# Kernel tuning notes

Measured on AMD Instinct MI355X. Metric: run time of the kernel, lower is better.

## Reference

```python
import jax, jax.numpy as jnp
import numpy as np

B = 1_000_000   # reflections
K = 16_384      # groups
E = 64          # encoder_out
H = 64          # hidden_dim


def setup_inputs() -> dict:
    key = jax.random.key(0)
    ks = jax.random.split(key, 12)
    x = jax.random.normal(ks[0], (B, E), dtype=jnp.float32)
    gl = jax.random.randint(ks[1], (B,), 0, K)
    # guarantee every group id 0..K-1 appears, so torch.unique == arange(K)
    gl = gl.at[:K].set(jnp.arange(K))
    s = 0.05
    W1 = jax.random.normal(ks[2], (E, H), jnp.float32) * s
    b1 = jax.random.normal(ks[3], (H,), jnp.float32) * s
    W2 = jax.random.normal(ks[4], (H, H), jnp.float32) * s
    b2 = jax.random.normal(ks[5], (H,), jnp.float32) * s
    W3 = jax.random.normal(ks[6], (H, H), jnp.float32) * s
    b3 = jax.random.normal(ks[7], (H,), jnp.float32) * s
    w_mu = jax.random.normal(ks[8], (H, 1), jnp.float32) * s
    b_mu = jnp.full((1,), -6.9, jnp.float32)   # log_tau_init
    w_lv = jax.random.normal(ks[9], (H, 1), jnp.float32) * s
    b_lv = jnp.full((1,), -2.0, jnp.float32)
    return {"x": x, "group_labels": gl, "W1": W1, "b1": b1, "W2": W2, "b2": b2,
            "W3": W3, "b3": b3, "w_mu": w_mu, "b_mu": b_mu, "w_lv": w_lv, "b_lv": b_lv}


def reference(x, group_labels, W1, b1, W2, b2, W3, b3, w_mu, b_mu, w_lv, b_lv):
    # phi: Linear -> SiLU -> Linear -> SiLU
    z = jax.nn.silu(jax.nn.silu(x @ W1 + b1) @ W2 + b2)          # (B, H)
    # segment mean by group (math-equivalent to the dense one-hot matmul)
    counts = jax.ops.segment_sum(jnp.ones((z.shape[0],), z.dtype),
                                 group_labels, num_segments=K)    # (K,)
    gsum = jax.ops.segment_sum(z, group_labels, num_segments=K)   # (K, H)
    group_features = gsum / counts[:, None]
    # rho + heads
    h = jax.nn.silu(group_features @ W3 + b3)                     # (K, H)
    mu = (h @ w_mu + b_mu)[:, 0]                                  # (K,)
    logvar = jnp.clip((h @ w_lv + b_lv)[:, 0], -10.0, 4.0)        # (K,)
    std = jnp.exp(0.5 * logvar)
    eps = jax.random.normal(jax.random.key(42), std.shape, std.dtype)
    log_tau = mu + std * eps                                      # reparam sample
    tau_group = jnp.exp(log_tau)
    # unique_groups == arange(K) by construction -> searchsorted is identity
    tau_per_refl = tau_group[group_labels][:, None]               # (B, 1)
    log_tau_per_refl = log_tau[group_labels][:, None]             # (B, 1)
    return (mu, logvar, tau_per_refl, log_tau_per_refl)
```

## Files before the change

### kernel.cpp

```cpp
#include <hip/hip_runtime.h>

#define BN 1000000
#define KN 16384
#define HN 64
#define TPB 512
#define NW  8
#define CHROWS 256
#define NB  512
#define NCHUNK ((BN + CHROWS - 1) / CHROWS)

typedef __bf16 bf16x8 __attribute__((ext_vector_type(8)));
typedef float  f32x4  __attribute__((ext_vector_type(4)));
typedef unsigned short u16x8 __attribute__((ext_vector_type(8)));

__device__ __forceinline__ unsigned short f2bf(float f) {
    return __builtin_bit_cast(unsigned short, (__bf16)f);
}
__device__ __forceinline__ float bf2f(unsigned short b) {
    return (float)__builtin_bit_cast(__bf16, b);
}
__device__ __forceinline__ float silu_f(float v) {
    return v * __builtin_amdgcn_rcpf(1.0f + __expf(-v));
}
__device__ __forceinline__ f32x4 mfma16(bf16x8 a, bf16x8 b, f32x4 c) {
    return __builtin_amdgcn_mfma_f32_16x16x32_bf16(a, b, c, 0, 0, 0);
}

__device__ __forceinline__ float erfinv_xla(float x) {
    float w = -log1pf(-x * x);
    float p;
    if (w < 5.0f) {
        w -= 2.5f;
        p = 2.81022636e-08f;
        p = fmaf(p, w, 3.43273939e-07f);
        p = fmaf(p, w, -3.5233877e-06f);
        p = fmaf(p, w, -4.39150654e-06f);
        p = fmaf(p, w, 0.00021858087f);
        p = fmaf(p, w, -0.00125372503f);
        p = fmaf(p, w, -0.00417768164f);
        p = fmaf(p, w, 0.246640727f);
        p = fmaf(p, w, 1.50140941f);
    } else {
        w = sqrtf(w) - 3.0f;
        p = -0.000200214257f;
        p = fmaf(p, w, 0.000100950558f);
        p = fmaf(p, w, 0.00134934322f);
        p = fmaf(p, w, -0.00367342844f);
        p = fmaf(p, w, 0.00573950773f);
        p = fmaf(p, w, -0.0076224613f);
        p = fmaf(p, w, 0.00943887047f);
        p = fmaf(p, w, 1.00167406f);
        p = fmaf(p, w, 2.83297682f);
    }
    return p * x;
}

__device__ __forceinline__ float jax_eps16384(int gid) {
    const unsigned k0 = 0u, k1 = 42u, k2 = 0x1BD11BDAu ^ 0u ^ 42u;
    unsigned x0 = 0u + k0;
    unsigned x1 = (unsigned)gid + k1;
#define TF_RND(r) { x0 += x1; x1 = (x1 << (r)) | (x1 >> (32 - (r))); x1 ^= x0; }
    TF_RND(13) TF_RND(15) TF_RND(26) TF_RND(6)  x0 += k1; x1 += k2 + 1u;
    TF_RND(17) TF_RND(29) TF_RND(16) TF_RND(24) x0 += k2; x1 += k0 + 2u;
    TF_RND(13) TF_RND(15) TF_RND(26) TF_RND(6)  x0 += k0; x1 += k1 + 3u;
    TF_RND(17) TF_RND(29) TF_RND(16) TF_RND(24) x0 += k1; x1 += k2 + 4u;
    TF_RND(13) TF_RND(15) TF_RND(26) TF_RND(6)  x0 += k2; x1 += k0 + 5u;
#undef TF_RND
    unsigned bits = x0 ^ x1;
    float f = __uint_as_float((bits >> 9) | 0x3f800000u) - 1.0f;
    const float mn = -0.99999994f;
    float u = fmaxf(f * 2.0f + mn, mn);
    return 1.41421354f * erfinv_xla(u);
}

__global__ __launch_bounds__(256) void k_count(const int* __restrict__ gl,
                                               int* __restrict__ counts,
                                               float4* __restrict__ gz) {
    int i = blockIdx.x * 256 + threadIdx.x;
    const float4 z4 = make_float4(0.f, 0.f, 0.f, 0.f);
    for (int j = i; j < KN * HN / 4; j += 250112) gz[j] = z4;
    if (i < BN / 4) {
        int4 g = ((const int4*)gl)[i];
        atomicAdd(&counts[g.x], 1); atomicAdd(&counts[g.y], 1);
        atomicAdd(&counts[g.z], 1); atomicAdd(&counts[g.w], 1);
    }
}

__global__ __launch_bounds__(1024) void k_scan(const int* __restrict__ counts, int* __restrict__ cursor) {
    __shared__ int wtot[16];
    const int t = threadIdx.x, lane = t & 63, wv = t >> 6;
    const int4* c4 = (const int4*)counts;
    int4 q0 = c4[t * 4], q1 = c4[t * 4 + 1], q2 = c4[t * 4 + 2], q3 = c4[t * 4 + 3];
    int c[16] = {q0.x, q0.y, q0.z, q0.w, q1.x, q1.y, q1.z, q1.w,
                 q2.x, q2.y, q2.z, q2.w, q3.x, q3.y, q3.z, q3.w};
    int loc[16], s = 0;
    #pragma unroll
    for (int i = 0; i < 16; ++i) { loc[i] = s; s += c[i]; }
    const int own = s;
    #pragma unroll
    for (int off = 1; off < 64; off <<= 1) {
        int v = __shfl_up(s, off);
        if (lane >= off) s += v;
    }
    if (lane == 63) wtot[wv] = s;
    __syncthreads();
    int wbase = 0;
    #pragma unroll
    for (int w = 0; w < 16; ++w) wbase += (w < wv) ? wtot[w] : 0;
    const int ebase = wbase + s - own;
    int o[16];
    #pragma unroll
    for (int i = 0; i < 16; ++i) o[i] = ebase + loc[i];
    int4* o4 = (int4*)cursor;
    o4[t * 4]     = make_int4(o[0],  o[1],  o[2],  o[3]);
    o4[t * 4 + 1] = make_int4(o[4],  o[5],  o[6],  o[7]);
    o4[t * 4 + 2] = make_int4(o[8],  o[9],  o[10], o[11]);
    o4[t * 4 + 3] = make_int4(o[12], o[13], o[14], o[15]);
}

__global__ __launch_bounds__(256) void k_scatter(const int* __restrict__ gl, int* __restrict__ cursor,
                                                 int2* __restrict__ spk) {
    int i = blockIdx.x * 256 + threadIdx.x;
    if (i < BN / 4) {
        int4 g = ((const int4*)gl)[i];
        int r = i * 4;
        int p0 = atomicAdd(&cursor[g.x], 1); spk[p0] = make_int2(r,     g.x);
        int p1 = atomicAdd(&cursor[g.y], 1); spk[p1] = make_int2(r + 1, g.y);
        int p2 = atomicAdd(&cursor[g.z], 1); spk[p2] = make_int2(r + 2, g.z);
        int p3 = atomicAdd(&cursor[g.w], 1); spk[p3] = make_int2(r + 3, g.w);
    }
}

__global__ __launch_bounds__(TPB, 4) void k_phase1(
    const float* __restrict__ x, const int2* __restrict__ spk,
    const float* __restrict__ W1, const float* __restrict__ b1,
    const float* __restrict__ W2, const float* __restrict__ b2,
    float* __restrict__ gsum)
{
    __shared__ __align__(16) unsigned short w1t[64 * 64];
    __shared__ __align__(16) unsigned short w2t[64 * 64];
    __shared__ __align__(16) unsigned short xh[NW][32 * 64];
    __shared__ float b1s[64], b2s[64];
    __shared__ int sg_s[NW][32];

    const int t = threadIdx.x;
    const int wv = t >> 6, lane = t & 63;
    const int lj = lane & 15, lg = lane >> 4;

    {
        const float4* W1v = (const float4*)W1;
        const float4* W2v = (const float4*)W2;
        #pragma unroll
        for (int i = 0; i < 2; ++i) {
            int e4 = i * TPB + t;
            int k  = e4 >> 4;
            int j0 = (e4 & 15) * 4;
            float4 a = W1v[e4];
            float4 b = W2v[e4];
            float av[4] = {a.x, a.y, a.z, a.w};
            float bv[4] = {b.x, b.y, b.z, b.w};
            #pragma unroll
            for (int c = 0; c < 4; ++c) {
                int j = j0 + c;
                int off = j * 128 + ((2 * k) ^ ((j & 7) << 4));
                *(unsigned short*)((char*)w1t + off) = f2bf(av[c]);
                *(unsigned short*)((char*)w2t + off) = f2bf(bv[c]);
            }
        }
        if (t < 64) { b1s[t] = b1[t]; b2s[t] = b2[t]; }
    }
    __syncthreads();

    float bc1[4], bc2[4];
    #pragma unroll
    for (int ct = 0; ct < 4; ++ct) { bc1[ct] = b1s[ct * 16 + lj]; bc2[ct] = b2s[ct * 16 + lj]; }

    unsigned short* myx = &xh[wv][0];
    int2 rsA[2], rsB[2];

    auto load_spk = [&](int c, int2 (&dst)[2]) {
        int cc = c < NCHUNK - 1 ? c : NCHUNK - 1;
        #pragma unroll
        for (int rt = 0; rt < 2; ++rt) {
            int r = cc * CHROWS + wv * 32 + rt * 16 + lj;
            dst[rt] = spk[r < BN ? r : BN - 1];
        }
    };

    auto iter = [&](int2 (&CUR)[2], int2 (&NXT)[2], int c) {
        float4 xr[2][4];
        #pragma unroll
        for (int rt = 0; rt < 2; ++rt) {
            const float* xp = x + (size_t)CUR[rt].x * 64 + lg * 8;
            xr[rt][0] = *(const float4*)(xp);
            xr[rt][1] = *(const float4*)(xp + 4);
            xr[rt][2] = *(const float4*)(xp + 32);
            xr[rt][3] = *(const float4*)(xp + 36);
        }
        load_spk(c + NB, NXT);
        if (lg == 0) {
            #pragma unroll
            for (int rt = 0; rt < 2; ++rt) {
                int r = c * CHROWS + wv * 32 + rt * 16 + lj;
                sg_s[wv][rt * 16 + lj] = (r < BN) ? CUR[rt].y : -1;
            }
        }
        bf16x8 af[2][2];
        #pragma unroll
        for (int rt = 0; rt < 2; ++rt)
            #pragma unroll
            for (int kk = 0; kk < 2; ++kk) {
                float4 a = xr[rt][kk * 2], b = xr[rt][kk * 2 + 1];
                u16x8 u;
                u[0] = f2bf(a.x); u[1] = f2bf(a.y); u[2] = f2bf(a.z); u[3] = f2bf(a.w);
                u[4] = f2bf(b.x); u[5] = f2bf(b.y); u[6] = f2bf(b.z); u[7] = f2bf(b.w);
                af[rt][kk] = __builtin_bit_cast(bf16x8, u);
            }

        f32x4 acc[2][4];
        #pragma unroll
        for (int a = 0; a < 2; ++a)
            #pragma unroll
            for (int b = 0; b < 4; ++b) acc[a][b] = f32x4{0.f, 0.f, 0.f, 0.f};
        #pragma unroll
        for (int kk = 0; kk < 2; ++kk) {
            const int kbyte = kk * 64 + lg * 16;
            bf16x8 bw[4];
            #pragma unroll
            for (int ct = 0; ct < 4; ++ct) {
                int row = ct * 16 + lj;
                bw[ct] = *(const bf16x8*)((char*)w1t + row * 128 + (kbyte ^ ((row & 7) << 4)));
            }
            #pragma unroll
            for (int rt = 0; rt < 2; ++rt)
                #pragma unroll
                for (int ct = 0; ct < 4; ++ct)
                    acc[rt][ct] = mfma16(af[rt][kk], bw[ct], acc[rt][ct]);
        }
        #pragma unroll
        for (int rt = 0; rt < 2; ++rt) {
            #pragma unroll
            for (int ct = 0; ct < 4; ++ct) {
                f32x4 v = acc[rt][ct];
                #pragma unroll
                for (int rg = 0; rg < 4; ++rg) {
                    int row = rt * 16 + lg * 4 + rg;
                    int col = ct * 16 + lj;
                    float h = silu_f(v[rg] + bc1[ct]);
                    int off = row * 128 + ((2 * col) ^ ((row & 7) << 4));
                    *(unsigned short*)((char*)myx + off) = f2bf(h);
                }
                acc[rt][ct] = f32x4{0.f, 0.f, 0.f, 0.f};
            }
        }
        #pragma unroll
        for (int kk = 0; kk < 2; ++kk) {
            const int kbyte = kk * 64 + lg * 16;
            bf16x8 bw[4];
            #pragma unroll
            for (int ct = 0; ct < 4; ++ct) {
                int row = ct * 16 + lj;
                bw[ct] = *(const bf16x8*)((char*)w2t + row * 128 + (kbyte ^ ((row & 7) << 4)));
            }
            #pragma unroll
            for (int rt = 0; rt < 2; ++rt) {
                int row = rt * 16 + lj;
                bf16x8 aw = *(const bf16x8*)((char*)myx + row * 128 + (kbyte ^ ((row & 7) << 4)));
                #pragma unroll
                for (int ct = 0; ct < 4; ++ct)
                    acc[rt][ct] = mfma16(aw, bw[ct], acc[rt][ct]);
            }
        }
        #pragma unroll
        for (int rt = 0; rt < 2; ++rt) {
            #pragma unroll
            for (int ct = 0; ct < 4; ++ct) {
                f32x4 v = acc[rt][ct];
                int col  = ct * 16 + lj;
                int row0 = rt * 16 + lg * 4;
                ushort4 pk;
                pk.x = f2bf(silu_f(v[0] + bc2[ct]));
                pk.y = f2bf(silu_f(v[1] + bc2[ct]));
                pk.z = f2bf(silu_f(v[2] + bc2[ct]));
                pk.w = f2bf(silu_f(v[3] + bc2[ct]));
                *(ushort4*)((char*)myx + col * 64 + ((2 * row0) ^ ((col & 3) << 4))) = pk;
            }
        }
        {
            const int c2 = lane;
            const char* zT = (const char*)myx;
            float vsum = 0.0f;
            int curg = -2;
            #pragma unroll
            for (int blk = 0; blk < 4; ++blk) {
                u16x8 v = *(const u16x8*)(zT + c2 * 64 + ((16 * blk) ^ ((c2 & 3) << 4)));
                int4 ga = *(const int4*)(&sg_s[wv][blk * 8]);
                int4 gb = *(const int4*)(&sg_s[wv][blk * 8 + 4]);
                int gs[8] = {ga.x, ga.y, ga.z, ga.w, gb.x, gb.y, gb.z, gb.w};
                #pragma unroll
                for (int j = 0; j < 8; ++j) {
                    int g = gs[j];
                    if (g != curg) {
                        if (curg >= 0) atomicAdd(&gsum[curg * 64 + c2], vsum);
                        vsum = 0.0f;
                        curg = g;
                    }
                    vsum += bf2f(v[j]);
                }
            }
            if (curg >= 0) atomicAdd(&gsum[curg * 64 + c2], vsum);
        }
    };

    int c = blockIdx.x;
    load_spk(c, rsA);
    while (true) {
        iter(rsA, rsB, c); c += NB; if (c >= NCHUNK) break;
        iter(rsB, rsA, c); c += NB; if (c >= NCHUNK) break;
    }
}

__global__ __launch_bounds__(64) void k_phase2(
    const float* __restrict__ gsum, const int* __restrict__ counts,
    const float* __restrict__ W3, const float* __restrict__ b3,
    const float* __restrict__ wmu, const float* __restrict__ bmu,
    const float* __restrict__ wlv, const float* __restrict__ blv,
    float* __restrict__ out, float* __restrict__ taug, float* __restrict__ ltaug)
{
    __shared__ __align__(16) float w3t[64 * 64];
    __shared__ float b3s[64], wmus[64], wlvs[64];
    const int t = threadIdx.x;
    for (int i = 0; i < 64; ++i) w3t[t * 64 + i] = W3[i * 64 + t];
    b3s[t] = b3[t]; wmus[t] = wmu[t]; wlvs[t] = wlv[t];
    __syncthreads();

    const int gid = blockIdx.x * 64 + t;
    const float inv = 1.0f / (float)counts[gid];
    float gf[64];
    #pragma unroll
    for (int i = 0; i < 16; ++i) {
        float4 v = *(const float4*)(gsum + (size_t)gid * 64 + i * 4);
        gf[i * 4 + 0] = v.x * inv; gf[i * 4 + 1] = v.y * inv;
        gf[i * 4 + 2] = v.z * inv; gf[i * 4 + 3] = v.w * inv;
    }
    float mu = bmu[0], lv = blv[0];
    for (int j = 0; j < 64; ++j) {
        float a = b3s[j];
        const float4* wr = (const float4*)(w3t + j * 64);
        #pragma unroll
        for (int k = 0; k < 16; ++k) {
            float4 wv = wr[k];
            a += gf[k * 4 + 0] * wv.x + gf[k * 4 + 1] * wv.y
               + gf[k * 4 + 2] * wv.z + gf[k * 4 + 3] * wv.w;
        }
        float h = silu_f(a);
        mu += h * wmus[j];
        lv += h * wlvs[j];
    }
    lv = fminf(fmaxf(lv, -10.0f), 4.0f);
    float sd  = __expf(0.5f * lv);
    float eps = jax_eps16384(gid);
    float lt  = mu + sd * eps;
    out[gid]      = mu;
    out[KN + gid] = lv;
    taug[gid]  = __expf(lt);
    ltaug[gid] = lt;
}

__global__ __launch_bounds__(256) void k_phase3(
    const int* __restrict__ gl, const float* __restrict__ taug,
    const float* __restrict__ ltaug, float* __restrict__ out)
{
    int i = blockIdx.x * 256 + threadIdx.x;
    if (i < BN / 4) {
        int4 g = ((const int4*)gl)[i];
        float4 tv = make_float4(taug[g.x],  taug[g.y],  taug[g.z],  taug[g.w]);
        float4 lv = make_float4(ltaug[g.x], ltaug[g.y], ltaug[g.z], ltaug[g.w]);
        ((float4*)(out + 2 * KN))[i]      = tv;
        ((float4*)(out + 2 * KN + BN))[i] = lv;
    }
}

extern "C" void kernel_launch(void* const* d_in, const int* in_sizes, int n_in,
                              void* d_out, int out_size, void* d_ws, size_t ws_size,
                              hipStream_t stream)
{
    const float* x   = (const float*)d_in[0];
    const int*   gl  = (const int*)d_in[1];
    const float* W1  = (const float*)d_in[2];
    const float* b1  = (const float*)d_in[3];
    const float* W2  = (const float*)d_in[4];
    const float* b2  = (const float*)d_in[5];
    const float* W3  = (const float*)d_in[6];
    const float* b3  = (const float*)d_in[7];
    const float* wmu = (const float*)d_in[8];
    const float* bmu = (const float*)d_in[9];
    const float* wlv = (const float*)d_in[10];
    const float* blv = (const float*)d_in[11];
    float* out = (float*)d_out;

    float* ws     = (float*)d_ws;
    float* gsum   = ws;
    int*   counts = (int*)(gsum + KN * HN);
    int*   cursor = counts + KN;
    float* taug   = (float*)(cursor + KN);
    float* ltaug  = taug + KN;
    int2*  spk    = (int2*)(ltaug + KN);

    hipMemsetAsync(counts, 0, (size_t)KN * sizeof(int), stream);

    const int nb4 = (BN / 4 + 255) / 256;
    k_count  <<<nb4, 256, 0, stream>>>(gl, counts, (float4*)gsum);
    k_scan   <<<1, 1024, 0, stream>>>(counts, cursor);
    k_scatter<<<nb4, 256, 0, stream>>>(gl, cursor, spk);
    k_phase1 <<<NB, TPB, 0, stream>>>(x, spk, W1, b1, W2, b2, gsum);
    k_phase2 <<<KN / 64, 64, 0, stream>>>(gsum, counts, W3, b3, wmu, bmu, wlv, blv, out, taug, ltaug);
    k_phase3 <<<nb4, 256, 0, stream>>>(gl, taug, ltaug, out);
}
```

Before: 233.8 us.

## Software-pipeline x row gathers one chunk ahead in phase1 MLP loop

Restructures the phase1 loop so the gathered x rows for the next chunk are loaded right after the current chunk's rows are converted to bf16, and sorted-index loads are prefetched two chunks ahead. Scheduling barriers pin these loads before the MFMA work so memory latency overlaps compute. It also reorders the weight fragment loads into pairs and reads biases from LDS instead of holding them in registers, to relieve register pressure. The cost is extra live registers for the prefetched x rows, which could hurt occupancy under the four-block launch bound.

```diff
diff --git a/kernel.cpp b/kernel.cpp
--- a/kernel.cpp
+++ b/kernel.cpp
@@ -2,11 +2,10 @@
 
 #define BN 1000000
 #define KN 16384
-#define HN 64
-#define TPB 512
-#define NW  8
+#define TPB1 512
+#define NW1 8
 #define CHROWS 256
-#define NB  512
+#define NB1 512
 #define NCHUNK ((BN + CHROWS - 1) / CHROWS)
 
 typedef __bf16 bf16x8 __attribute__((ext_vector_type(8)));
@@ -78,7 +77,7 @@
                                                float4* __restrict__ gz) {
     int i = blockIdx.x * 256 + threadIdx.x;
     const float4 z4 = make_float4(0.f, 0.f, 0.f, 0.f);
-    for (int j = i; j < KN * HN / 4; j += 250112) gz[j] = z4;
+    for (int j = i; j < KN * 64 / 4; j += 250112) gz[j] = z4;
     if (i < BN / 4) {
         int4 g = ((const int4*)gl)[i];
         atomicAdd(&counts[g.x], 1); atomicAdd(&counts[g.y], 1);
@@ -131,7 +130,7 @@
     }
 }
 
-__global__ __launch_bounds__(TPB, 4) void k_phase1(
+__global__ __launch_bounds__(TPB1, 4) void k_phase1(
     const float* __restrict__ x, const int2* __restrict__ spk,
     const float* __restrict__ W1, const float* __restrict__ b1,
     const float* __restrict__ W2, const float* __restrict__ b2,
@@ -139,9 +138,9 @@
 {
     __shared__ __align__(16) unsigned short w1t[64 * 64];
     __shared__ __align__(16) unsigned short w2t[64 * 64];
-    __shared__ __align__(16) unsigned short xh[NW][32 * 64];
+    __shared__ __align__(16) unsigned short xh[NW1][32 * 64];
     __shared__ float b1s[64], b2s[64];
-    __shared__ int sg_s[NW][32];
+    __shared__ int sg_s[NW1][32];
 
     const int t = threadIdx.x;
     const int wv = t >> 6, lane = t & 63;
@@ -152,7 +151,7 @@
         const float4* W2v = (const float4*)W2;
         #pragma unroll
         for (int i = 0; i < 2; ++i) {
-            int e4 = i * TPB + t;
+            int e4 = i * TPB1 + t;
             int k  = e4 >> 4;
             int j0 = (e4 & 15) * 4;
             float4 a = W1v[e4];
@@ -171,12 +170,9 @@
     }
     __syncthreads();
 
-    float bc1[4], bc2[4];
-    #pragma unroll
-    for (int ct = 0; ct < 4; ++ct) { bc1[ct] = b1s[ct * 16 + lj]; bc2[ct] = b2s[ct * 16 + lj]; }
-
     unsigned short* myx = &xh[wv][0];
-    int2 rsA[2], rsB[2];
+    int2   rsA[2], rsB[2];
+    float4 xr[2][4];
 
     auto load_spk = [&](int c, int2 (&dst)[2]) {
         int cc = c < NCHUNK - 1 ? c : NCHUNK - 1;
@@ -186,25 +182,18 @@
             dst[rt] = spk[r < BN ? r : BN - 1];
         }
     };
-
-    auto iter = [&](int2 (&CUR)[2], int2 (&NXT)[2], int c) {
-        float4 xr[2][4];
+    auto load_x = [&](const int2 (&src)[2]) {
         #pragma unroll
         for (int rt = 0; rt < 2; ++rt) {
-            const float* xp = x + (size_t)CUR[rt].x * 64 + lg * 8;
+            const float* xp = x + (size_t)src[rt].x * 64 + lg * 8;
             xr[rt][0] = *(const float4*)(xp);
             xr[rt][1] = *(const float4*)(xp + 4);
             xr[rt][2] = *(const float4*)(xp + 32);
             xr[rt][3] = *(const float4*)(xp + 36);
         }
-        load_spk(c + NB, NXT);
-        if (lg == 0) {
-            #pragma unroll
-            for (int rt = 0; rt < 2; ++rt) {
-                int r = c * CHROWS + wv * 32 + rt * 16 + lj;
-                sg_s[wv][rt * 16 + lj] = (r < BN) ? CUR[rt].y : -1;
-            }
-        }
+    };
+
+    auto iter = [&](int2 (&CUR)[2], int2 (&NXT)[2], int c) {
         bf16x8 af[2][2];
         #pragma unroll
         for (int rt = 0; rt < 2; ++rt)
@@ -216,6 +205,17 @@
                 u[4] = f2bf(b.x); u[5] = f2bf(b.y); u[6] = f2bf(b.z); u[7] = f2bf(b.w);
                 af[rt][kk] = __builtin_bit_cast(bf16x8, u);
             }
+        if (lg == 0) {
+            #pragma unroll
+            for (int rt = 0; rt < 2; ++rt) {
+                int r = c * CHROWS + wv * 32 + rt * 16 + lj;
+                sg_s[wv][rt * 16 + lj] = (r < BN) ? CUR[rt].y : -1;
+            }
+        }
+        __builtin_amdgcn_sched_barrier(0);
+        load_x(NXT);
+        load_spk(c + 2 * NB1, CUR);
+        __builtin_amdgcn_sched_barrier(0);
 
         f32x4 acc[2][4];
         #pragma unroll
@@ -225,28 +225,29 @@
         #pragma unroll
         for (int kk = 0; kk < 2; ++kk) {
             const int kbyte = kk * 64 + lg * 16;
-            bf16x8 bw[4];
+            #pragma unroll
+            for (int cth = 0; cth < 2; ++cth) {
+                int r0 = (cth * 2) * 16 + lj, r1 = (cth * 2 + 1) * 16 + lj;
+                bf16x8 bw0 = *(const bf16x8*)((char*)w1t + r0 * 128 + (kbyte ^ ((r0 & 7) << 4)));
+                bf16x8 bw1 = *(const bf16x8*)((char*)w1t + r1 * 128 + (kbyte ^ ((r1 & 7) << 4)));
+                #pragma unroll
+                for (int rt = 0; rt < 2; ++rt) {
+                    acc[rt][cth * 2]     = mfma16(af[rt][kk], bw0, acc[rt][cth * 2]);
+                    acc[rt][cth * 2 + 1] = mfma16(af[rt][kk], bw1, acc[rt][cth * 2 + 1]);
+                }
+            }
+        }
+        #pragma unroll
+        for (int rt = 0; rt < 2; ++rt) {
             #pragma unroll
             for (int ct = 0; ct < 4; ++ct) {
-                int row = ct * 16 + lj;
-                bw[ct] = *(const bf16x8*)((char*)w1t + row * 128 + (kbyte ^ ((row & 7) << 4)));
-            }
-            #pragma unroll
-            for (int rt = 0; rt < 2; ++rt)
-                #pragma unroll
-                for (int ct = 0; ct < 4; ++ct)
-                    acc[rt][ct] = mfma16(af[rt][kk], bw[ct], acc[rt][ct]);
-        }
-        #pragma unroll
-        for (int rt = 0; rt < 2; ++rt) {
-            #pragma unroll
-            for (int ct = 0; ct < 4; ++ct) {
+                float bc = b1s[ct * 16 + lj];
                 f32x4 v = acc[rt][ct];
                 #pragma unroll
                 for (int rg = 0; rg < 4; ++rg) {
                     int row = rt * 16 + lg * 4 + rg;
                     int col = ct * 16 + lj;
-                    float h = silu_f(v[rg] + bc1[ct]);
+                    float h = silu_f(v[rg] + bc);
                     int off = row * 128 + ((2 * col) ^ ((row & 7) << 4));
                     *(unsigned short*)((char*)myx + off) = f2bf(h);
                 }
@@ -256,33 +257,33 @@
         #pragma unroll
         for (int kk = 0; kk < 2; ++kk) {
             const int kbyte = kk * 64 + lg * 16;
-            bf16x8 bw[4];
+            #pragma unroll
+            for (int cth = 0; cth < 2; ++cth) {
+                int r0 = (cth * 2) * 16 + lj, r1 = (cth * 2 + 1) * 16 + lj;
+                bf16x8 bw0 = *(const bf16x8*)((char*)w2t + r0 * 128 + (kbyte ^ ((r0 & 7) << 4)));
+                bf16x8 bw1 = *(const bf16x8*)((char*)w2t + r1 * 128 + (kbyte ^ ((r1 & 7) << 4)));
+                #pragma unroll
+                for (int rt = 0; rt < 2; ++rt) {
+                    int row = rt * 16 + lj;
+                    bf16x8 aw = *(const bf16x8*)((char*)myx + row * 128 + (kbyte ^ ((row & 7) << 4)));
+                    acc[rt][cth * 2]     = mfma16(aw, bw0, acc[rt][cth * 2]);
+                    acc[rt][cth * 2 + 1] = mfma16(aw, bw1, acc[rt][cth * 2 + 1]);
+                }
+            }
+        }
+        #pragma unroll
+        for (int rt = 0; rt < 2; ++rt) {
             #pragma unroll
             for (int ct = 0; ct < 4; ++ct) {
-                int row = ct * 16 + lj;
-                bw[ct] = *(const bf16x8*)((char*)w2t + row * 128 + (kbyte ^ ((row & 7) << 4)));
-            }
-            #pragma unroll
-            for (int rt = 0; rt < 2; ++rt) {
-                int row = rt * 16 + lj;
-                bf16x8 aw = *(const bf16x8*)((char*)myx + row * 128 + (kbyte ^ ((row & 7) << 4)));
-                #pragma unroll
-                for (int ct = 0; ct < 4; ++ct)
-                    acc[rt][ct] = mfma16(aw, bw[ct], acc[rt][ct]);
-            }
-        }
-        #pragma unroll
-        for (int rt = 0; rt < 2; ++rt) {
-            #pragma unroll
-            for (int ct = 0; ct < 4; ++ct) {
+                float bc = b2s[ct * 16 + lj];
                 f32x4 v = acc[rt][ct];
                 int col  = ct * 16 + lj;
                 int row0 = rt * 16 + lg * 4;
                 ushort4 pk;
-                pk.x = f2bf(silu_f(v[0] + bc2[ct]));
-                pk.y = f2bf(silu_f(v[1] + bc2[ct]));
-                pk.z = f2bf(silu_f(v[2] + bc2[ct]));
-                pk.w = f2bf(silu_f(v[3] + bc2[ct]));
+                pk.x = f2bf(silu_f(v[0] + bc));
+                pk.y = f2bf(silu_f(v[1] + bc));
+                pk.z = f2bf(silu_f(v[2] + bc));
+                pk.w = f2bf(silu_f(v[3] + bc));
                 *(ushort4*)((char*)myx + col * 64 + ((2 * row0) ^ ((col & 3) << 4))) = pk;
             }
         }
@@ -314,9 +315,11 @@
 
     int c = blockIdx.x;
     load_spk(c, rsA);
+    load_x(rsA);
+    load_spk(c + NB1, rsB);
     while (true) {
-        iter(rsA, rsB, c); c += NB; if (c >= NCHUNK) break;
-        iter(rsB, rsA, c); c += NB; if (c >= NCHUNK) break;
+        iter(rsA, rsB, c); c += NB1; if (c >= NCHUNK) break;
+        iter(rsB, rsA, c); c += NB1; if (c >= NCHUNK) break;
     }
 }
 
@@ -401,7 +404,7 @@
 
     float* ws     = (float*)d_ws;
     float* gsum   = ws;
-    int*   counts = (int*)(gsum + KN * HN);
+    int*   counts = (int*)(gsum + KN * 64);
     int*   cursor = counts + KN;
     float* taug   = (float*)(cursor + KN);
     float* ltaug  = taug + KN;
@@ -413,7 +416,7 @@
     k_count  <<<nb4, 256, 0, stream>>>(gl, counts, (float4*)gsum);
     k_scan   <<<1, 1024, 0, stream>>>(counts, cursor);
     k_scatter<<<nb4, 256, 0, stream>>>(gl, cursor, spk);
-    k_phase1 <<<NB, TPB, 0, stream>>>(x, spk, W1, b1, W2, b2, gsum);
+    k_phase1 <<<NB1, TPB1, 0, stream>>>(x, spk, W1, b1, W2, b2, gsum);
     k_phase2 <<<KN / 64, 64, 0, stream>>>(gsum, counts, W3, b3, wmu, bmu, wlv, blv, out, taug, ltaug);
     k_phase3 <<<nb4, 256, 0, stream>>>(gl, taug, ltaug, out);
 }
```

Measured after the change: 275.9 us. 18.0% more time.
